# Optimization experiments

Hardware: AMD Instinct MI355X
Metric: run time of the kernel (lower is better)

The kernel has to match this reference:

```python
import jax, jax.numpy as jnp
import numpy as np

INPUT_SIZE = 512
HIDDEN_SIZE = 512
BATCH = 128
SEQ_LEN = 512


def setup_inputs() -> dict:
    key = jax.random.key(0)
    k_xs, k_wih, k_whh, k_b, k_bn = jax.random.split(key, 5)
    lim = 1.0 / np.sqrt(HIDDEN_SIZE)  # equinox GRUCell init: U(-1/sqrt(H), 1/sqrt(H))
    xs = jax.random.normal(k_xs, (BATCH, SEQ_LEN, INPUT_SIZE), dtype=jnp.float32)
    weight_ih = jax.random.uniform(k_wih, (3 * HIDDEN_SIZE, INPUT_SIZE), minval=-lim, maxval=lim, dtype=jnp.float32)
    weight_hh = jax.random.uniform(k_whh, (3 * HIDDEN_SIZE, HIDDEN_SIZE), minval=-lim, maxval=lim, dtype=jnp.float32)
    bias = jax.random.uniform(k_b, (3 * HIDDEN_SIZE,), minval=-lim, maxval=lim, dtype=jnp.float32)
    bias_n = jax.random.uniform(k_bn, (HIDDEN_SIZE,), minval=-lim, maxval=lim, dtype=jnp.float32)
    return {"xs": xs, "weight_ih": weight_ih, "weight_hh": weight_hh, "bias": bias, "bias_n": bias_n}


def _gru_scan(xs, weight_ih, weight_hh, bias, bias_n):
    # xs: [B, T, I]. Precompute all input-side gates in one big GEMM: [B, T, 3H]
    igates_all = jnp.einsum('bti,gi->btg', xs, weight_ih) + bias
    B = xs.shape[0]
    H = weight_hh.shape[1]

    def step(h, ig_t):  # h: [B, H], ig_t: [B, 3H]
        hg = h @ weight_hh.T  # [B, 3H]
        ir, iz, in_ = jnp.split(ig_t, 3, axis=-1)
        hr, hz, hn = jnp.split(hg, 3, axis=-1)
        r = jax.nn.sigmoid(ir + hr)
        z = jax.nn.sigmoid(iz + hz)
        n = jnp.tanh(in_ + r * (hn + bias_n))
        h_new = n + z * (h - n)  # equinox GRUCell: new + inp*(hidden - new)
        return h_new, None

    init = jnp.zeros((B, H), dtype=xs.dtype)
    final_state, _ = jax.lax.scan(step, init, jnp.swapaxes(igates_all, 0, 1))  # scan over T
    return final_state  # [B, H]


def reference(xs, weight_ih, weight_hh, bias, bias_n):
    return _gru_scan(xs, weight_ih, weight_hh, bias, bias_n)
```

## Files before the change

### kernel.cpp

```cpp
#include <hip/hip_runtime.h>
#include <hip/hip_bf16.h>
#include <stdint.h>


static constexpr int INPUT = 512;
static constexpr int HID   = 512;
static constexpr int NB    = 128;
static constexpr int TLEN  = 512;
static constexpr int BGRPS = 8;
static constexpr int UGRPS = 32;

typedef __attribute__((ext_vector_type(4))) float f32x4;
typedef __attribute__((ext_vector_type(8))) short s16x8;

static __device__ __forceinline__ unsigned short f2bf(float f) {
  unsigned u = __builtin_bit_cast(unsigned, f);
  u += 0x7FFFu + ((u >> 16) & 1u);
  return (unsigned short)(u >> 16);
}

static __device__ __forceinline__ s16x8 cvt8(const float* p) {
  f32x4 a = *(const f32x4*)p;
  f32x4 b = *(const f32x4*)(p + 4);
  s16x8 r;
  r[0] = (short)f2bf(a[0]); r[1] = (short)f2bf(a[1]);
  r[2] = (short)f2bf(a[2]); r[3] = (short)f2bf(a[3]);
  r[4] = (short)f2bf(b[0]); r[5] = (short)f2bf(b[1]);
  r[6] = (short)f2bf(b[2]); r[7] = (short)f2bf(b[3]);
  return r;
}

__global__ __launch_bounds__(192, 2) void gru_fused(
    const float* __restrict__ xs, const float* __restrict__ wih,
    const float* __restrict__ whh, const float* __restrict__ bias,
    const float* __restrict__ bias_n, float* __restrict__ out,
    unsigned short* __restrict__ hbuf, unsigned int* __restrict__ cnt)
{
  const int wg   = blockIdx.x;
  const int bgrp = wg & 7;
  const int ugrp = wg >> 3;
  const int b0   = bgrp * 16;
  const int u0   = ugrp * 16;
  const int tid  = threadIdx.x;
  const int g    = tid >> 6;
  const int lane = tid & 63;
  const int ln   = lane & 15;
  const int kg   = lane >> 4;

  const int rowW = g * HID + u0 + ln;
  s16x8 wa[16], wb[16];
#pragma unroll
  for (int ks = 0; ks < 16; ++ks) {
    const int k = ks * 32 + kg * 8;
    wa[ks] = cvt8(wih + (size_t)rowW * INPUT + k);
    wb[ks] = cvt8(whh + (size_t)rowW * HID + k);
  }
  const float bv = bias[rowW];
  const float bn = bias_n[u0 + ln];

  const float* xrow = xs + (size_t)(b0 + ln) * TLEN * INPUT + kg * 8;
  const int hoff = (b0 + ln) * HID + kg * 8;

  __shared__ float xch[4][16][16];

  float hold[4] = {0.f, 0.f, 0.f, 0.f};

  f32x4 acc_a = {bv, bv, bv, bv};
#pragma unroll
  for (int ks = 0; ks < 16; ++ks) {
    s16x8 xa = cvt8(xrow + ks * 32);
    acc_a = __builtin_amdgcn_mfma_f32_16x16x32_bf16(xa, wa[ks], acc_a, 0, 0, 0);
  }

  for (int t = 0; t < TLEN; ++t) {
    if (t > 0) {
      if (tid == 0) {
        while (__hip_atomic_load(&cnt[(t - 1) * BGRPS + bgrp],
                                 __ATOMIC_RELAXED, __HIP_MEMORY_SCOPE_AGENT) < (unsigned)UGRPS) {}
      }
      __syncthreads();
      __builtin_amdgcn_sched_barrier(0);
    }

    const unsigned long long* hb =
        (const unsigned long long*)(hbuf + (size_t)(t & 1) * (NB * HID) + hoff);
    unsigned long long q0[16], q1[16];
#pragma unroll
    for (int ks = 0; ks < 16; ++ks) {
      q0[ks] = __hip_atomic_load(hb + ks * 8,     __ATOMIC_RELAXED, __HIP_MEMORY_SCOPE_AGENT);
      q1[ks] = __hip_atomic_load(hb + ks * 8 + 1, __ATOMIC_RELAXED, __HIP_MEMORY_SCOPE_AGENT);
    }
    f32x4 acc_b0 = {0.f, 0.f, 0.f, 0.f}, acc_b1 = {0.f, 0.f, 0.f, 0.f};
#pragma unroll
    for (int ks = 0; ks < 16; ks += 2) {
      union { unsigned long long q[2]; s16x8 s; } ua, ub;
      ua.q[0] = q0[ks];     ua.q[1] = q1[ks];
      ub.q[0] = q0[ks + 1]; ub.q[1] = q1[ks + 1];
      acc_b0 = __builtin_amdgcn_mfma_f32_16x16x32_bf16(ua.s, wb[ks],     acc_b0, 0, 0, 0);
      acc_b1 = __builtin_amdgcn_mfma_f32_16x16x32_bf16(ub.s, wb[ks + 1], acc_b1, 0, 0, 0);
    }
    f32x4 acc_b = acc_b0 + acc_b1;

    if (g == 0)      { f32x4 s = acc_a + acc_b; *(f32x4*)&xch[0][ln][kg * 4] = s; }
    else if (g == 1) { f32x4 s = acc_a + acc_b; *(f32x4*)&xch[1][ln][kg * 4] = s; }
    else             { *(f32x4*)&xch[2][ln][kg * 4] = acc_a;
                       *(f32x4*)&xch[3][ln][kg * 4] = acc_b; }
    __syncthreads();
    f32x4 Sr  = *(const f32x4*)&xch[0][ln][kg * 4];
    f32x4 Sz  = *(const f32x4*)&xch[1][ln][kg * 4];
    f32x4 Snx = *(const f32x4*)&xch[2][ln][kg * 4];
    f32x4 Snh = *(const f32x4*)&xch[3][ln][kg * 4];

    float hnew[4];
#pragma unroll
    for (int i = 0; i < 4; ++i) {
      float r = 1.f / (1.f + __expf(-Sr[i]));
      float z = 1.f / (1.f + __expf(-Sz[i]));
      float pre = Snx[i] + r * (Snh[i] + bn);
      float e = __expf(2.f * pre);
      float n = 1.f - 2.f / (e + 1.f);
      hnew[i] = n + z * (hold[i] - n);
      hold[i] = hnew[i];
    }

    if (t == TLEN - 1) {
      if (g == 0) {
#pragma unroll
        for (int i = 0; i < 4; ++i)
          out[(size_t)(b0 + kg * 4 + i) * HID + u0 + ln] = hnew[i];
      }
    } else {
      if (g == 0) {
        unsigned short* hbn = hbuf + (size_t)((t + 1) & 1) * (NB * HID);
#pragma unroll
        for (int i = 0; i < 4; ++i) {
          int v  = (int)f2bf(hnew[i]);
          int o1 = __shfl_xor(v, 1);
          unsigned int p = (unsigned int)(v & 0xffff) | ((unsigned int)(o1 & 0xffff) << 16);
          unsigned int o2 = (unsigned int)__shfl_xor((int)p, 2);
          if ((ln & 3) == 0) {
            unsigned long long q = (unsigned long long)p | ((unsigned long long)o2 << 32);
            __hip_atomic_store(
                (unsigned long long*)(hbn + (size_t)(b0 + kg * 4 + i) * HID + u0 + ln),
                q, __ATOMIC_RELAXED, __HIP_MEMORY_SCOPE_AGENT);
          }
        }
        asm volatile("s_waitcnt vmcnt(0)" ::: "memory");
        if (tid == 0)
          __hip_atomic_fetch_add(&cnt[t * BGRPS + bgrp], 1u,
                                 __ATOMIC_RELAXED, __HIP_MEMORY_SCOPE_AGENT);
      }

      acc_a = (f32x4){bv, bv, bv, bv};
      const float* xp = xrow + (size_t)(t + 1) * INPUT;
#pragma unroll
      for (int ks = 0; ks < 16; ++ks) {
        s16x8 xa = cvt8(xp + ks * 32);
        acc_a = __builtin_amdgcn_mfma_f32_16x16x32_bf16(xa, wa[ks], acc_a, 0, 0, 0);
      }
    }
  }
}

extern "C" void kernel_launch(void* const* d_in, const int* in_sizes, int n_in,
                              void* d_out, int out_size, void* d_ws, size_t ws_size,
                              hipStream_t stream) {
  const float* xs     = (const float*)d_in[0];
  const float* wih    = (const float*)d_in[1];
  const float* whh    = (const float*)d_in[2];
  const float* bias   = (const float*)d_in[3];
  const float* bias_n = (const float*)d_in[4];
  float* out = (float*)d_out;

  const size_t hbuf_bytes = (size_t)2 * NB * HID * sizeof(unsigned short);
  const size_t cnt_bytes  = (size_t)TLEN * BGRPS * sizeof(unsigned int);
  unsigned short* hbuf = (unsigned short*)d_ws;
  unsigned int*   cnt  = (unsigned int*)((char*)d_ws + hbuf_bytes);

  hipMemsetAsync(d_ws, 0, hbuf_bytes + cnt_bytes, stream);

  gru_fused<<<dim3(BGRPS * UGRPS), dim3(192), 0, stream>>>(
      xs, wih, whh, bias, bias_n, out, hbuf, cnt);
}
```

Measured before the change: 4.169 ms.

## Replace atomic counter barrier with per-producer step flags polled by every wave

Replaces the per-step atomic counter, where one thread spins and then does a workgroup __syncthreads, with per-workgroup flags storing the last completed step. Each wave polls all 32 producer flags of its batch group with a ballot and proceeds without a block-wide barrier. The LDS exchange buffer is double-buffered by step parity so that dropping the barrier is still safe. This removes one __syncthreads and the contended fetch_add from every step, at the cost of every wave hammering 32 flag words and relying on relaxed ordering for visibility of the h data.

```diff
diff --git a/kernel.cpp b/kernel.cpp
--- a/kernel.cpp
+++ b/kernel.cpp
@@ -34,7 +34,7 @@
     const float* __restrict__ xs, const float* __restrict__ wih,
     const float* __restrict__ whh, const float* __restrict__ bias,
     const float* __restrict__ bias_n, float* __restrict__ out,
-    unsigned short* __restrict__ hbuf, unsigned int* __restrict__ cnt)
+    unsigned short* __restrict__ hbuf, unsigned int* __restrict__ flags)
 {
   const int wg   = blockIdx.x;
   const int bgrp = wg & 7;
@@ -61,7 +61,7 @@
   const float* xrow = xs + (size_t)(b0 + ln) * TLEN * INPUT + kg * 8;
   const int hoff = (b0 + ln) * HID + kg * 8;
 
-  __shared__ float xch[4][16][16];
+  __shared__ float xch[2][4][16][16];
 
   float hold[4] = {0.f, 0.f, 0.f, 0.f};
 
@@ -74,11 +74,11 @@
 
   for (int t = 0; t < TLEN; ++t) {
     if (t > 0) {
-      if (tid == 0) {
-        while (__hip_atomic_load(&cnt[(t - 1) * BGRPS + bgrp],
-                                 __ATOMIC_RELAXED, __HIP_MEMORY_SCOPE_AGENT) < (unsigned)UGRPS) {}
-      }
-      __syncthreads();
+      const unsigned* fp = &flags[bgrp * UGRPS + (lane & 31)];
+      unsigned fv;
+      do {
+        fv = __hip_atomic_load(fp, __ATOMIC_RELAXED, __HIP_MEMORY_SCOPE_AGENT);
+      } while (~__ballot(fv >= (unsigned)t));
       __builtin_amdgcn_sched_barrier(0);
     }
 
@@ -90,6 +90,7 @@
       q0[ks] = __hip_atomic_load(hb + ks * 8,     __ATOMIC_RELAXED, __HIP_MEMORY_SCOPE_AGENT);
       q1[ks] = __hip_atomic_load(hb + ks * 8 + 1, __ATOMIC_RELAXED, __HIP_MEMORY_SCOPE_AGENT);
     }
+
     f32x4 acc_b0 = {0.f, 0.f, 0.f, 0.f}, acc_b1 = {0.f, 0.f, 0.f, 0.f};
 #pragma unroll
     for (int ks = 0; ks < 16; ks += 2) {
@@ -101,15 +102,16 @@
     }
     f32x4 acc_b = acc_b0 + acc_b1;
 
-    if (g == 0)      { f32x4 s = acc_a + acc_b; *(f32x4*)&xch[0][ln][kg * 4] = s; }
-    else if (g == 1) { f32x4 s = acc_a + acc_b; *(f32x4*)&xch[1][ln][kg * 4] = s; }
-    else             { *(f32x4*)&xch[2][ln][kg * 4] = acc_a;
-                       *(f32x4*)&xch[3][ln][kg * 4] = acc_b; }
+    float (*xc)[16][16] = xch[t & 1];
+    if (g == 0)      { f32x4 s = acc_a + acc_b; *(f32x4*)&xc[0][ln][kg * 4] = s; }
+    else if (g == 1) { f32x4 s = acc_a + acc_b; *(f32x4*)&xc[1][ln][kg * 4] = s; }
+    else             { *(f32x4*)&xc[2][ln][kg * 4] = acc_a;
+                       *(f32x4*)&xc[3][ln][kg * 4] = acc_b; }
     __syncthreads();
-    f32x4 Sr  = *(const f32x4*)&xch[0][ln][kg * 4];
-    f32x4 Sz  = *(const f32x4*)&xch[1][ln][kg * 4];
-    f32x4 Snx = *(const f32x4*)&xch[2][ln][kg * 4];
-    f32x4 Snh = *(const f32x4*)&xch[3][ln][kg * 4];
+    f32x4 Sr  = *(const f32x4*)&xc[0][ln][kg * 4];
+    f32x4 Sz  = *(const f32x4*)&xc[1][ln][kg * 4];
+    f32x4 Snx = *(const f32x4*)&xc[2][ln][kg * 4];
+    f32x4 Snh = *(const f32x4*)&xc[3][ln][kg * 4];
 
     float hnew[4];
 #pragma unroll
@@ -147,8 +149,8 @@
         }
         asm volatile("s_waitcnt vmcnt(0)" ::: "memory");
         if (tid == 0)
-          __hip_atomic_fetch_add(&cnt[t * BGRPS + bgrp], 1u,
-                                 __ATOMIC_RELAXED, __HIP_MEMORY_SCOPE_AGENT);
+          __hip_atomic_store(&flags[bgrp * UGRPS + ugrp], (unsigned)(t + 1),
+                             __ATOMIC_RELAXED, __HIP_MEMORY_SCOPE_AGENT);
       }
 
       acc_a = (f32x4){bv, bv, bv, bv};
@@ -173,12 +175,12 @@
   float* out = (float*)d_out;
 
   const size_t hbuf_bytes = (size_t)2 * NB * HID * sizeof(unsigned short);
-  const size_t cnt_bytes  = (size_t)TLEN * BGRPS * sizeof(unsigned int);
-  unsigned short* hbuf = (unsigned short*)d_ws;
-  unsigned int*   cnt  = (unsigned int*)((char*)d_ws + hbuf_bytes);
+  const size_t flg_bytes  = (size_t)BGRPS * UGRPS * sizeof(unsigned int);
+  unsigned short* hbuf  = (unsigned short*)d_ws;
+  unsigned int*   flags = (unsigned int*)((char*)d_ws + hbuf_bytes);
 
-  hipMemsetAsync(d_ws, 0, hbuf_bytes + cnt_bytes, stream);
+  hipMemsetAsync(d_ws, 0, hbuf_bytes + flg_bytes, stream);
 
   gru_fused<<<dim3(BGRPS * UGRPS), dim3(192), 0, stream>>>(
-      xs, wih, whh, bias, bias_n, out, hbuf, cnt);
+      xs, wih, whh, bias, bias_n, out, hbuf, flags);
 }
```

Measured after the change: 3.553 ms. 1.17x faster.
